# Optimization experiments

Hardware: AMD Instinct MI355X
Metric: run time of the kernel (lower is better)

## Reference

```python
import jax, jax.numpy as jnp
from jax import lax
import numpy as np

B, L, D_MODEL = 4, 2048, 1024
D_INNER = 2 * D_MODEL          # expand=2
N = 16                          # d_state
DCONV = 4                       # d_conv
DTRANK = D_MODEL // 16          # dt_rank = 64
DFF = 4 * D_MODEL               # 4096


def setup_inputs() -> dict:
    key = jax.random.key(0)
    ks = jax.random.split(key, 10)
    def g(i, shape, scale=0.02):
        return jax.random.normal(ks[i], shape, jnp.float32) * scale
    return {
        "x": jax.random.normal(ks[0], (B, L, D_MODEL), jnp.float32),
        # Mamba params (mamba_ssm defaults: in_proj/x_proj/out_proj no bias)
        "in_proj_w": g(1, (2 * D_INNER, D_MODEL)),
        "conv_w": g(2, (D_INNER, 1, DCONV), 0.1),
        "conv_b": jnp.zeros((D_INNER,), jnp.float32),
        "x_proj_w": g(3, (DTRANK + 2 * N, D_INNER)),
        "dt_proj_w": g(4, (D_INNER, DTRANK), 0.1),
        # inverse-softplus of ~0.01 so softplus(dt) starts small, as in Mamba init
        "dt_proj_b": jnp.log(jnp.expm1(jnp.full((D_INNER,), 1e-2, jnp.float32))),
        "A_log": jnp.log(jnp.broadcast_to(jnp.arange(1, N + 1, dtype=jnp.float32), (D_INNER, N))),
        "D": jnp.ones((D_INNER,), jnp.float32),
        "out_proj_w": g(5, (D_MODEL, D_INNER)),
        # FFN params (nn.Linear has bias)
        "lin1_w": g(6, (DFF, D_MODEL)),
        "lin1_b": jnp.zeros((DFF,), jnp.float32),
        "lin2_w": g(7, (D_MODEL, DFF)),
        "lin2_b": jnp.zeros((D_MODEL,), jnp.float32),
    }


def _mamba(x, in_proj_w, conv_w, conv_b, x_proj_w, dt_proj_w, dt_proj_b,
           A_log, D, out_proj_w):
    Bb = x.shape[0]
    xz = jnp.einsum('bld,ed->ble', x, in_proj_w)        # [B,L,2*d_inner]
    u, z = jnp.split(xz, 2, axis=-1)                    # each [B,L,d_inner]
    # causal depthwise conv1d over time
    uc = jnp.transpose(u, (0, 2, 1))                    # [B,d_inner,L]
    uc = lax.conv_general_dilated(uc, conv_w, (1,), [(DCONV - 1, 0)],
                                  feature_group_count=D_INNER)
    uc = jax.nn.silu(uc + conv_b[None, :, None])
    u = jnp.transpose(uc, (0, 2, 1))                    # [B,L,d_inner]
    # input-dependent dt, B, C
    x_dbl = jnp.einsum('ble,fe->blf', u, x_proj_w)      # [B,L,dt_rank+2N]
    dt, Bm, Cm = jnp.split(x_dbl, [DTRANK, DTRANK + N], axis=-1)
    dt = jax.nn.softplus(jnp.einsum('blr,er->ble', dt, dt_proj_w) + dt_proj_b)
    A = -jnp.exp(A_log)                                 # [d_inner,N]

    def step(h, inputs):
        u_t, dt_t, B_t, C_t = inputs                    # [B,E],[B,E],[B,N],[B,N]
        dA = jnp.exp(dt_t[..., None] * A)               # [B,E,N]
        h = dA * h + (dt_t * u_t)[..., None] * B_t[:, None, :]
        y = jnp.einsum('ben,bn->be', h, C_t)
        return h, y

    h0 = jnp.zeros((Bb, D_INNER, N), x.dtype)
    xs = (jnp.transpose(u, (1, 0, 2)), jnp.transpose(dt, (1, 0, 2)),
          jnp.transpose(Bm, (1, 0, 2)), jnp.transpose(Cm, (1, 0, 2)))
    _, ys = lax.scan(step, h0, xs)                      # ys: [L,B,d_inner]
    y = jnp.transpose(ys, (1, 0, 2)) + u * D
    y = y * jax.nn.silu(z)
    return jnp.einsum('ble,de->bld', y, out_proj_w)     # [B,L,d_model]


def reference(x, in_proj_w, conv_w, conv_b, x_proj_w, dt_proj_w, dt_proj_b,
              A_log, D, out_proj_w, lin1_w, lin1_b, lin2_w, lin2_b):
    y = _mamba(x, in_proj_w, conv_w, conv_b, x_proj_w, dt_proj_w, dt_proj_b,
               A_log, D, out_proj_w)
    h = jax.nn.relu(jnp.einsum('bld,fd->blf', y, lin1_w) + lin1_b)
    return jnp.einsum('blf,df->bld', h, lin2_w) + lin2_b
```

## Files before the change

### kernel.cpp

```cpp
#include <hip/hip_runtime.h>
#include <hip/hip_bf16.h>
#include <type_traits>
#include <math.h>

typedef __hip_bfloat16 bf16_t;

#define BB 4
#define LL 2048
#define DM 1024
#define DI 2048
#define NS 16
#define DTR 64
#define DFF 4096
#define MTOK (BB*LL)
#define NC 32
#define CL (LL/NC)
#define TT 16
#define KS 4

#if defined(__has_builtin)
#if __has_builtin(__builtin_amdgcn_exp2f)
#define EXP2F(x) __builtin_amdgcn_exp2f(x)
#endif
#endif
#ifndef EXP2F
#define EXP2F(x) exp2f(x)
#endif
#define LOG2E 1.44269504088896340736f

__device__ __forceinline__ float b2f_lo(unsigned u) {
    union { unsigned x; float f; } c; c.x = u << 16; return c.f;
}
__device__ __forceinline__ float b2f_hi(unsigned u) {
    union { unsigned x; float f; } c; c.x = u & 0xffff0000u; return c.f;
}
__device__ __forceinline__ void unpack8(uint4 v, float* o) {
    o[0] = b2f_lo(v.x); o[1] = b2f_hi(v.x);
    o[2] = b2f_lo(v.y); o[3] = b2f_hi(v.y);
    o[4] = b2f_lo(v.z); o[5] = b2f_hi(v.z);
    o[6] = b2f_lo(v.w); o[7] = b2f_hi(v.w);
}

typedef __attribute__((ext_vector_type(8))) short bf16x8;
typedef __attribute__((ext_vector_type(4))) float f32x4;

__device__ __forceinline__ void gld_lds16(const void* g, void* l) {
    __builtin_amdgcn_global_load_lds(
        (const __attribute__((address_space(1))) void*)g,
        (__attribute__((address_space(3))) void*)l, 16, 0, 0);
}

#define G8_BAR  __builtin_amdgcn_s_barrier()
#define G8_SB   __builtin_amdgcn_sched_barrier(0)
#define G8_LGKM do { asm volatile("s_waitcnt lgkmcnt(0)" ::: "memory"); G8_SB; } while (0)
#define G8_VM8  do { asm volatile("s_waitcnt vmcnt(8)"   ::: "memory"); G8_SB; } while (0)
#define G8_VM6  do { asm volatile("s_waitcnt vmcnt(6)"   ::: "memory"); G8_SB; } while (0)
#define G8_VM4  do { asm volatile("s_waitcnt vmcnt(4)"   ::: "memory"); G8_SB; } while (0)
#define G8_VM2  do { asm volatile("s_waitcnt vmcnt(2)"   ::: "memory"); G8_SB; } while (0)
#define G8_VM0  do { asm volatile("s_waitcnt vmcnt(0)"   ::: "memory"); G8_SB; } while (0)

__global__ void detect_dtype_kernel(const unsigned* __restrict__ x, int* __restrict__ flag)
{
    __shared__ int cnt;
    if (threadIdx.x == 0) cnt = 0;
    __syncthreads();
    int c = 0;
    for (int i = threadIdx.x; i < 4096; i += 256) {
        unsigned w = x[i];
        int e = (w >> 7) & 0xFF;
        c += (e >= 100 && e <= 140) ? 1 : 0;
    }
    atomicAdd(&cnt, c);
    __syncthreads();
    if (threadIdx.x == 0) *flag = (cnt > 2048) ? 1 : 0;
}

struct CvtDesc {
    const void* src[14];
    bf16_t*     dst[14];
    int         cum[15];
};

__global__ __launch_bounds__(256)
void convert_all(CvtDesc d, const int* __restrict__ flag, int total8)
{
    int i = blockIdx.x * 256 + threadIdx.x;
    if (i >= total8) return;
    int t = 0;
#pragma unroll 1
    while (i >= d.cum[t + 1]) ++t;
    int j = i - d.cum[t];
    if (*flag) {
        ((uint4*)d.dst[t])[j] = ((const uint4*)d.src[t])[j];
    } else {
        const float4* s = (const float4*)d.src[t] + (size_t)j * 2;
        float4 a = s[0], b = s[1];
        bf16_t o[8];
        o[0] = __float2bfloat16(a.x); o[1] = __float2bfloat16(a.y);
        o[2] = __float2bfloat16(a.z); o[3] = __float2bfloat16(a.w);
        o[4] = __float2bfloat16(b.x); o[5] = __float2bfloat16(b.y);
        o[6] = __float2bfloat16(b.z); o[7] = __float2bfloat16(b.w);
        ((uint4*)d.dst[t])[j] = *(uint4*)o;
    }
}

#define G8_NK 16

template <int EPI, bool SPLIT>
__global__ __launch_bounds__(512, 2)
void gemm8(const bf16_t* __restrict__ A, const bf16_t* __restrict__ W,
           bf16_t* __restrict__ C, bf16_t* __restrict__ C2,
           const bf16_t* __restrict__ bias, int ldc)
{
    __shared__ __align__(16) bf16_t ldsmem[2][2][256 * 64];

    const int tid  = threadIdx.x;
    const int lane = tid & 63;
    const int wv   = tid >> 6;
    const int wm   = wv >> 2;
    const int wn   = wv & 3;
    const int r16  = lane & 15;
    const int q    = lane >> 4;
    const int m0   = blockIdx.x * 256;
    const int n0   = blockIdx.y * 256;

    const int x0 = q ^ (r16 & 7);
    const int x1 = (4 + q) ^ (r16 & 7);

    const int srow = tid >> 3;
    const int scol = (tid & 7) ^ (srow & 7);
    const bf16_t* Abase = A + (size_t)(m0 + srow) * 1024 + scol * 8;
    const bf16_t* Wbase = W + (size_t)(n0 + srow) * 1024 + scol * 8;
    const int woff = wv * 1024;

    const bf16x8* L8 = (const bf16x8*)ldsmem;
    char*         Lb = (char*)ldsmem;

    f32x4  acc[8][4] = {};
    bf16x8 af[4][2];
    bf16x8 bfr[2][2][2];

    auto stA = [&](int bufc, int tile, int half) {
        const bf16_t* g = Abase + (size_t)half * (128 * 1024) + tile * 64;
        char* l = Lb + (size_t)(bufc * 2 + 0) * 32768 + half * 16384 + woff;
        gld_lds16(g, l);
        gld_lds16(g + 64 * 1024, l + 8192);
    };
    auto stB = [&](int bufc, int tile, int half) {
        const bf16_t* g = Wbase + (size_t)half * (128 * 1024) + tile * 64;
        char* l = Lb + (size_t)(bufc * 2 + 1) * 32768 + half * 16384 + woff;
        gld_lds16(g, l);
        gld_lds16(g + 64 * 1024, l + 8192);
    };
    auto rdA = [&](int bufc, int mh) {
#pragma unroll
        for (int mf = 0; mf < 4; ++mf) {
            int rb = (bufc * 2 + 0) * 2048 + (wm * 128 + mh * 64 + mf * 16 + r16) * 8;
            af[mf][0] = L8[rb + x0];
            af[mf][1] = L8[rb + x1];
        }
    };
    auto rdB = [&](int bufc, int nh) {
#pragma unroll
        for (int nf = 0; nf < 2; ++nf) {
            int rb = (bufc * 2 + 1) * 2048 + (wn * 64 + nh * 32 + nf * 16 + r16) * 8;
            bfr[nh][nf][0] = L8[rb + x0];
            bfr[nh][nf][1] = L8[rb + x1];
        }
    };
    auto mmQ = [&](int mh, int nh) {
#pragma unroll
        for (int mf = 0; mf < 4; ++mf)
#pragma unroll
            for (int nf = 0; nf < 2; ++nf) {
                acc[mh*4+mf][nh*2+nf] = __builtin_amdgcn_mfma_f32_16x16x32_bf16(
                    af[mf][0], bfr[nh][nf][0], acc[mh*4+mf][nh*2+nf], 0, 0, 0);
                acc[mh*4+mf][nh*2+nf] = __builtin_amdgcn_mfma_f32_16x16x32_bf16(
                    af[mf][1], bfr[nh][nf][1], acc[mh*4+mf][nh*2+nf], 0, 0, 0);
            }
    };

#define G8_PH(mh, nh) do { G8_BAR; G8_LGKM;                      \
        __builtin_amdgcn_s_setprio(1); mmQ(mh, nh);              \
        __builtin_amdgcn_s_setprio(0); G8_SB; G8_BAR; G8_SB; } while (0)

    stA(0, 0, 0); stA(0, 0, 1);
    stB(0, 0, 0); stB(0, 0, 1);
    stB(1, 1, 0); stB(1, 1, 1);
    G8_VM4;
    G8_BAR; G8_SB;

    for (int i = 0; i < G8_NK / 2 - 1; ++i) {
        const int v1 = 2 * i + 1, u2 = 2 * i + 2, v2 = 2 * i + 3;
        rdA(0,0); rdB(0,0); stA(1, v1, 0);         G8_PH(0,0);
        rdB(0,1);           stA(1, v1, 1);         G8_PH(0,1);
        rdA(0,1);           stB(0, u2, 0);         G8_PH(1,0);
                            stB(0, u2, 1); G8_VM4; G8_PH(1,1);
        rdA(1,0); rdB(1,0); stA(0, u2, 0);         G8_PH(0,0);
        rdB(1,1);           stA(0, u2, 1);         G8_PH(0,1);
        rdA(1,1);           stB(1, v2, 0);         G8_PH(1,0);
                            stB(1, v2, 1); G8_VM4; G8_PH(1,1);
    }
    rdA(0,0); rdB(0,0); stA(1, G8_NK - 1, 0); G8_PH(0,0);
    rdB(0,1);           stA(1, G8_NK - 1, 1); G8_PH(0,1);
    rdA(0,1);                                 G8_PH(1,0);
                        G8_VM0;               G8_PH(1,1);
    rdA(1,0); rdB(1,0);                       G8_PH(0,0);
    rdB(1,1);                                 G8_PH(0,1);
    rdA(1,1);                                 G8_PH(1,0);
                                              G8_PH(1,1);

    bf16_t* Cb = C;
    int csub = 0;
    if (SPLIT && n0 >= 2048) { Cb = C2; csub = 2048; }
#pragma unroll
    for (int b = 0; b < 4; ++b) {
        int colg = n0 + wn * 64 + (b >> 1) * 32 + (b & 1) * 16 + r16;
        float bv = 0.f;
        if (EPI >= 1) bv = __bfloat162float(bias[colg]);
#pragma unroll
        for (int a = 0; a < 8; ++a) {
#pragma unroll
            for (int r = 0; r < 4; ++r) {
                int rowg = m0 + wm * 128 + (a >> 2) * 64 + (a & 3) * 16 + q * 4 + r;
                float v = acc[a][b][r];
                if (EPI >= 1) v += bv;
                if (EPI == 2) v = v > 0.f ? v : 0.f;
                Cb[(size_t)rowg * ldc + (colg - csub)] = __float2bfloat16(v);
            }
        }
    }
#undef G8_PH
}

template <int LDK, int NKT, int EPI, bool DYN>
__global__ __launch_bounds__(512, 2)
void gemm8n(const bf16_t* __restrict__ A, const bf16_t* __restrict__ W,
            bf16_t* __restrict__ C, const bf16_t* __restrict__ bias, int ldc,
            const int* oflag, int c_row_off)
{
    __shared__ __align__(16) bf16_t ldsmem[2][24576];

    const int tid  = threadIdx.x;
    const int lane = tid & 63;
    const int wv   = tid >> 6;
    const int wm   = wv >> 2;
    const int wn   = wv & 3;
    const int r16  = lane & 15;
    const int q    = lane >> 4;
    const int m0   = blockIdx.x * 256;
    const int n0   = blockIdx.y * 128;

    const int x0 = q ^ (r16 & 7);
    const int x1 = (4 + q) ^ (r16 & 7);

    const int srow = tid >> 3;
    const int scol = (tid & 7) ^ (srow & 7);
    const bf16_t* Abase = A + (size_t)(m0 + srow) * LDK + scol * 8;
    const bf16_t* Wbase = W + (size_t)(n0 + srow) * LDK + scol * 8;
    const int woff = wv * 1024;

    const bf16x8* L8 = (const bf16x8*)ldsmem;
    char*         Lb = (char*)ldsmem;

    f32x4  acc[8][2] = {};
    bf16x8 af[4][2];
    bf16x8 bfr[2][2];

    auto stA = [&](int bufc, int tile, int half) {
        const bf16_t* g = Abase + (size_t)half * (128 * LDK) + tile * 64;
        char* l = Lb + (size_t)bufc * 49152 + half * 16384 + woff;
        gld_lds16(g, l);
        gld_lds16(g + (size_t)64 * LDK, l + 8192);
    };
    auto stB = [&](int bufc, int tile) {
        const bf16_t* g = Wbase + tile * 64;
        char* l = Lb + (size_t)bufc * 49152 + 32768 + woff;
        gld_lds16(g, l);
        gld_lds16(g + (size_t)64 * LDK, l + 8192);
    };
    auto rdA = [&](int bufc, int mh) {
#pragma unroll
        for (int mf = 0; mf < 4; ++mf) {
            int rb = bufc * 3072 + (wm * 128 + mh * 64 + mf * 16 + r16) * 8;
            af[mf][0] = L8[rb + x0];
            af[mf][1] = L8[rb + x1];
        }
    };
    auto rdB = [&](int bufc) {
#pragma unroll
        for (int nf = 0; nf < 2; ++nf) {
            int rb = bufc * 3072 + 2048 + (wn * 32 + nf * 16 + r16) * 8;
            bfr[nf][0] = L8[rb + x0];
            bfr[nf][1] = L8[rb + x1];
        }
    };
    auto mmP = [&](int mh) {
#pragma unroll
        for (int mf = 0; mf < 4; ++mf)
#pragma unroll
            for (int nf = 0; nf < 2; ++nf) {
                acc[mh*4+mf][nf] = __builtin_amdgcn_mfma_f32_16x16x32_bf16(
                    af[mf][0], bfr[nf][0], acc[mh*4+mf][nf], 0, 0, 0);
                acc[mh*4+mf][nf] = __builtin_amdgcn_mfma_f32_16x16x32_bf16(
                    af[mf][1], bfr[nf][1], acc[mh*4+mf][nf], 0, 0, 0);
            }
    };

#define GN_PH(mh) do { G8_BAR; G8_LGKM;                          \
        __builtin_amdgcn_s_setprio(1); mmP(mh);                  \
        __builtin_amdgcn_s_setprio(0); G8_SB; G8_BAR; G8_SB; } while (0)

    stA(0, 0, 0); stA(0, 0, 1);
    stB(0, 0);
    stB(1, 1);
    G8_VM2;
    G8_BAR; G8_SB;

    for (int i = 0; i < NKT / 2 - 1; ++i) {
        const int v1 = 2 * i + 1, u2 = 2 * i + 2, v2 = 2 * i + 3;
        rdA(0,0); rdB(0); stA(1, v1, 0); stA(1, v1, 1); GN_PH(0);
        rdA(0,1);         stB(0, u2); G8_VM2;           GN_PH(1);
        rdA(1,0); rdB(1); stA(0, u2, 0); stA(0, u2, 1); GN_PH(0);
        rdA(1,1);         stB(1, v2); G8_VM2;           GN_PH(1);
    }
    rdA(0,0); rdB(0); stA(1, NKT - 1, 0); stA(1, NKT - 1, 1); GN_PH(0);
    rdA(0,1);         G8_VM0;                                 GN_PH(1);
    rdA(1,0); rdB(1);                                         GN_PH(0);
    rdA(1,1);                                                 GN_PH(1);

    int of = 1;
    if constexpr (DYN) of = *oflag;
#pragma unroll
    for (int nf = 0; nf < 2; ++nf) {
        int colg = n0 + wn * 32 + nf * 16 + r16;
        float bv = 0.f;
        if (EPI >= 1) bv = __bfloat162float(bias[colg]);
#pragma unroll
        for (int a = 0; a < 8; ++a) {
#pragma unroll
            for (int r = 0; r < 4; ++r) {
                int rowg = m0 + wm * 128 + a * 16 + q * 4 + r;
                float v = acc[a][nf][r];
                if (EPI >= 1) v += bv;
                if constexpr (DYN) {
                    size_t idx = (size_t)(c_row_off + rowg) * ldc + colg;
                    if (of) ((bf16_t*)C)[idx] = __float2bfloat16(v);
                    else    ((float*)C)[idx]  = v;
                } else {
                    C[(size_t)rowg * ldc + colg] = __float2bfloat16(v);
                }
            }
        }
    }
#undef GN_PH
}

#define TM 128
#define TN 128
#define TK 64

template <typename OutT, int EPI, bool DYN, bool EDGE>
__global__ __launch_bounds__(256, 2)
void gemm_bt(const bf16_t* __restrict__ A, int lda,
             const bf16_t* __restrict__ W, int ldw,
             OutT* __restrict__ C, int ldc,
             OutT* __restrict__ C2, int nsplit,
             const bf16_t* __restrict__ bias,
             int M, int N, int K,
             const int* oflag, int c_row_off)
{
    __shared__ bf16_t sA[TM * TK];
    __shared__ bf16_t sB[TN * TK];

    const int tid  = threadIdx.x;
    const int lane = tid & 63;
    const int wv   = tid >> 6;
    const int m0   = blockIdx.x * TM;
    const int n0   = blockIdx.y * TN;
    const int wm   = (wv >> 1) * 64;
    const int wn   = (wv & 1) * 64;
    const int r16  = lane & 15;
    const int q    = lane >> 4;

    int of = 1;
    if constexpr (DYN) of = *oflag;

    f32x4 acc[4][4] = {};

    for (int k0 = 0; k0 < K; k0 += TK) {
#pragma unroll
        for (int i = 0; i < 4; ++i) {
            int c    = (i * 4 + wv) * 64 + lane;
            int row  = c >> 3;
            int col8 = c & 7;
            const bf16_t* ga = A + (size_t)(m0 + row) * lda + k0 + col8 * 8;
            gld_lds16(ga, (char*)sA + (size_t)(i * 4 + wv) * 1024);
            int nrow = n0 + row;
            if (EDGE && nrow > N - 1) nrow = N - 1;
            const bf16_t* gb = W + (size_t)nrow * ldw + k0 + col8 * 8;
            gld_lds16(gb, (char*)sB + (size_t)(i * 4 + wv) * 1024);
        }
        __syncthreads();

        const bf16x8* sA8 = (const bf16x8*)sA;
        const bf16x8* sB8 = (const bf16x8*)sB;
#pragma unroll
        for (int kk = 0; kk < 2; ++kk) {
            bf16x8 af[4], bfr[4];
#pragma unroll
            for (int i = 0; i < 4; ++i)
                af[i] = sA8[(wm + i * 16 + r16) * 8 + kk * 4 + q];
#pragma unroll
            for (int j = 0; j < 4; ++j)
                bfr[j] = sB8[(wn + j * 16 + r16) * 8 + kk * 4 + q];
#pragma unroll
            for (int i = 0; i < 4; ++i)
#pragma unroll
                for (int j = 0; j < 4; ++j)
                    acc[i][j] = __builtin_amdgcn_mfma_f32_16x16x32_bf16(
                        af[i], bfr[j], acc[i][j], 0, 0, 0);
        }
        __syncthreads();
    }

    OutT* Cb = C;
    int csub = 0;
    if (C2 != nullptr && n0 >= nsplit) { Cb = C2; csub = nsplit; }

#pragma unroll
    for (int j = 0; j < 4; ++j) {
        int colg = n0 + wn + j * 16 + r16;
        if (EDGE && colg >= N) continue;
        float bv = 0.f;
        if (EPI >= 1) bv = __bfloat162float(bias[colg]);
#pragma unroll
        for (int i = 0; i < 4; ++i) {
#pragma unroll
            for (int r = 0; r < 4; ++r) {
                int rowg = m0 + wm + i * 16 + q * 4 + r;
                if (EDGE && rowg >= M) continue;
                float v = acc[i][j][r];
                if (EPI >= 1) v += bv;
                if (EPI == 2) v = v > 0.f ? v : 0.f;
                if (EPI == 3) v = (v > 20.f) ? v : log1pf(__expf(v));
                if constexpr (DYN) {
                    size_t idx = (size_t)(c_row_off + rowg) * ldc + colg;
                    if (of) ((bf16_t*)Cb)[idx] = __float2bfloat16(v);
                    else    ((float*)Cb)[idx]  = v;
                } else if constexpr (std::is_same<OutT, float>::value) {
                    Cb[(size_t)rowg * ldc + (colg - csub)] = v;
                } else {
                    Cb[(size_t)rowg * ldc + (colg - csub)] = __float2bfloat16(v);
                }
            }
        }
    }
}

__global__ __launch_bounds__(256, 2)
void gemm_xproj_splitk(const bf16_t* __restrict__ A,
                       const bf16_t* __restrict__ W,
                       float* __restrict__ part, int M)
{
    __shared__ bf16_t sA[TM * TK];
    __shared__ bf16_t sB[TN * TK];

    const int tid  = threadIdx.x;
    const int lane = tid & 63;
    const int wv   = tid >> 6;
    const int m0   = blockIdx.x * TM;
    const int kz   = blockIdx.z;
    const int wm   = (wv >> 1) * 64;
    const int wn   = (wv & 1) * 64;
    const int r16  = lane & 15;
    const int q    = lane >> 4;

    f32x4 acc[4][4] = {};

    const int kbeg = kz * (2048 / KS);
    for (int k0 = kbeg; k0 < kbeg + 2048 / KS; k0 += TK) {
#pragma unroll
        for (int i = 0; i < 4; ++i) {
            int c    = (i * 4 + wv) * 64 + lane;
            int row  = c >> 3;
            int col8 = c & 7;
            const bf16_t* ga = A + (size_t)(m0 + row) * DI + k0 + col8 * 8;
            gld_lds16(ga, (char*)sA + (size_t)(i * 4 + wv) * 1024);
            int nrow = row; if (nrow > 95) nrow = 95;
            const bf16_t* gb = W + (size_t)nrow * DI + k0 + col8 * 8;
            gld_lds16(gb, (char*)sB + (size_t)(i * 4 + wv) * 1024);
        }
        __syncthreads();

        const bf16x8* sA8 = (const bf16x8*)sA;
        const bf16x8* sB8 = (const bf16x8*)sB;
#pragma unroll
        for (int kk = 0; kk < 2; ++kk) {
            bf16x8 af[4], bfr[4];
#pragma unroll
            for (int i = 0; i < 4; ++i)
                af[i] = sA8[(wm + i * 16 + r16) * 8 + kk * 4 + q];
#pragma unroll
            for (int j = 0; j < 4; ++j)
                bfr[j] = sB8[(wn + j * 16 + r16) * 8 + kk * 4 + q];
#pragma unroll
            for (int i = 0; i < 4; ++i)
#pragma unroll
                for (int j = 0; j < 4; ++j)
                    acc[i][j] = __builtin_amdgcn_mfma_f32_16x16x32_bf16(
                        af[i], bfr[j], acc[i][j], 0, 0, 0);
        }
        __syncthreads();
    }

#pragma unroll
    for (int j = 0; j < 4; ++j) {
        int colg = wn + j * 16 + r16;
        if (colg >= 96) continue;
#pragma unroll
        for (int i = 0; i < 4; ++i) {
#pragma unroll
            for (int r = 0; r < 4; ++r) {
                int rowg = m0 + wm + i * 16 + q * 4 + r;
                part[((size_t)kz * M + rowg) * 96 + colg] = acc[i][j][r];
            }
        }
    }
}

__global__ __launch_bounds__(256)
void xproj_reduce(const float* __restrict__ part, bf16_t* __restrict__ xdbl,
                  float* __restrict__ x32, int M)
{
    int i = blockIdx.x * 256 + threadIdx.x;
    int n = M * 96;
    if (i >= n) return;
    float s = part[i] + part[(size_t)n + i] + part[2 * (size_t)n + i] + part[3 * (size_t)n + i];
    xdbl[i] = __float2bfloat16(s);
    if (x32) x32[i] = s;
}

__global__ __launch_bounds__(256)
void conv_silu_kernel(const bf16_t* __restrict__ u,
                      const bf16_t* __restrict__ cw,
                      const bf16_t* __restrict__ cb,
                      bf16_t* __restrict__ uc,
                      int Mrows)
{
    int idx = blockIdx.x * 256 + threadIdx.x;
    int eg  = idx & 255;
    int row = idx >> 8;
    if (row >= Mrows) return;
    int t = row & (LL - 1);
    int b = row >> 11;
    int e0 = eg * 8;

    float wf[32];
    {
        const uint4* wp = (const uint4*)(cw + (size_t)e0 * 4);
        uint4 w0 = wp[0], w1 = wp[1], w2 = wp[2], w3 = wp[3];
        unpack8(w0, wf); unpack8(w1, wf + 8); unpack8(w2, wf + 16); unpack8(w3, wf + 24);
    }
    float bias[8];
    unpack8(*(const uint4*)(cb + e0), bias);

    float uk[4][8];
#pragma unroll
    for (int k = 0; k < 4; ++k) {
        int tt = t - 3 + k;
        if (tt >= 0) {
            uint4 uv = *(const uint4*)(u + (size_t)(b * LL + tt) * DI + e0);
            unpack8(uv, uk[k]);
        } else {
#pragma unroll
            for (int j = 0; j < 8; ++j) uk[k][j] = 0.f;
        }
    }
    bf16_t out8[8];
#pragma unroll
    for (int j = 0; j < 8; ++j) {
        float a = bias[j];
#pragma unroll
        for (int k = 0; k < 4; ++k) a += wf[j * 4 + k] * uk[k][j];
        a = a / (1.f + __expf(-a));
        out8[j] = __float2bfloat16(a);
    }
    *(uint4*)(uc + (size_t)row * DI + e0) = *(uint4*)out8;
}


__global__ __launch_bounds__(256, 4)
void scan_pass1(const bf16_t* __restrict__ uc, const bf16_t* __restrict__ dtb,
                const float* __restrict__ x32, const bf16_t* __restrict__ A_log,
                float* __restrict__ hfin, float* __restrict__ Ssum, int lgG)
{
    __shared__ __align__(16) char sm1[36864];
    const int tid  = threadIdx.x;
    const int lane = tid & 63;
    const int wv   = tid >> 6;
    const int bid  = blockIdx.x;
    const int eb   = bid & 7;
    const int rem  = bid >> 3;
    const int b    = rem & ((1 << lgG) - 1);
    const int chunk = rem >> lgG;
    const int e0   = eb * 256;
    const int e    = e0 + tid;
    const int t0   = chunk * CL;

    const bf16_t* ub = uc  + (size_t)(b * LL + t0) * DI;
    const bf16_t* db = dtb + (size_t)(b * LL + t0) * DI;
    const float*  xr = x32 + (size_t)(b * LL + t0) * 96 + 64;

    char* const U[2] = { sm1, sm1 + 8192 };
    char* const D[2] = { sm1 + 16384, sm1 + 24576 };
    char* const Bl   = sm1 + 32768;

    auto stage2 = [&](const bf16_t* src, char* dst, int trow0) {
        const int c8 = (lane & 31) * 8;
        const int r0 = 2 * wv + (lane >> 5);
        gld_lds16(src + (size_t)(trow0 + r0) * DI + e0 + c8, dst + wv * 1024 + lane * 16);
        gld_lds16(src + (size_t)(trow0 + r0 + 8) * DI + e0 + c8, dst + (wv + 4) * 1024 + lane * 16);
    };
    {
        int s = tid >> 2, p = tid & 3;
        gld_lds16(xr + (size_t)s * 96 + p * 4, Bl + tid * 16);
    }
    stage2(ub, U[0], 0);  stage2(db, D[0], 0);
    stage2(ub, U[1], TT); stage2(db, D[1], TT);

    float alf[16];
    {
        uint4 v0 = *(const uint4*)(A_log + (size_t)e * NS);
        uint4 v1 = *(const uint4*)(A_log + (size_t)e * NS + 8);
        unpack8(v0, alf); unpack8(v1, alf + 8);
    }
    float a0 = -__expf(alf[0]) * LOG2E;
    float Aa2[16];
    int fast = 1;
#pragma unroll
    for (int n = 0; n < 16; ++n) {
        Aa2[n] = -__expf(alf[n]) * LOG2E;
        float ideal = (float)(n + 1) * a0;
        fast = fast && (fabsf(Aa2[n] - ideal) <= 0.02f * fabsf(ideal));
    }
    int allfast = __syncthreads_and(fast);

    float h[16];
#pragma unroll
    for (int j = 0; j < 16; ++j) h[j] = 0.f;
    float Ss = 0.f;

#define P1_CMP(K, FAST) do {                                                  \
        const char* Ut = U[(K) & 1]; const char* Dt = D[(K) & 1];             \
        _Pragma("unroll")                                                     \
        for (int t = 0; t < TT; ++t) {                                        \
            float cu  = __bfloat162float(*(const bf16_t*)(Ut + t * 512 + tid * 2)); \
            float cdt = __bfloat162float(*(const bf16_t*)(Dt + t * 512 + tid * 2)); \
            const float* bc = (const float*)(Bl + ((K) * TT + t) * 64);       \
            float du = cdt * cu; Ss += cdt;                                   \
            if (FAST) {                                                       \
                float r = EXP2F(cdt * a0);                                    \
                float r2 = r * r, r4 = r2 * r2, r8 = r4 * r4;                 \
                float dA = r, dB = r8 * r;                                    \
                _Pragma("unroll")                                             \
                for (int j = 0; j < 8; ++j) { h[j] = dA * h[j] + du * bc[j]; dA *= r; } \
                _Pragma("unroll")                                             \
                for (int j = 8; j < 16; ++j) { h[j] = dB * h[j] + du * bc[j]; dB *= r; } \
            } else {                                                          \
                _Pragma("unroll")                                             \
                for (int j = 0; j < 16; ++j) {                                \
                    float dA = EXP2F(cdt * Aa2[j]);                           \
                    h[j] = dA * h[j] + du * bc[j]; }                          \
            }                                                                 \
        } } while (0)

#define P1_SEQ(FAST) do {                                                     \
        G8_VM4; G8_BAR; G8_SB;                                                \
        P1_CMP(0, FAST); G8_LGKM; G8_BAR; G8_SB;                              \
        stage2(ub, U[0], 2 * TT); stage2(db, D[0], 2 * TT);                   \
        G8_VM4; G8_BAR; G8_SB;                                                \
        P1_CMP(1, FAST); G8_LGKM; G8_BAR; G8_SB;                              \
        stage2(ub, U[1], 3 * TT); stage2(db, D[1], 3 * TT);                   \
        G8_VM4; G8_BAR; G8_SB;                                                \
        P1_CMP(2, FAST); G8_LGKM; G8_BAR; G8_SB;                              \
        G8_VM0; G8_BAR; G8_SB;                                                \
        P1_CMP(3, FAST);                                                      \
    } while (0)

    if (allfast) P1_SEQ(true); else P1_SEQ(false);
#undef P1_SEQ
#undef P1_CMP

    size_t base = (size_t)(b * NC + chunk) * NS * DI + e;
#pragma unroll
    for (int j = 0; j < 16; ++j) hfin[base + (size_t)j * DI] = h[j];
    Ssum[(size_t)(b * NC + chunk) * DI + e] = Ss;
}

__global__ __launch_bounds__(256)
void scan_pass2(const float* __restrict__ Ssum, const bf16_t* __restrict__ A_log,
                float* __restrict__ hfin)
{
    int idx = blockIdx.x * 256 + threadIdx.x;
    int e = idx & (DI - 1);
    int rem = idx >> 11;
    int n = rem & (NS - 1);
    int b = rem >> 4;
    float Aa2 = -__expf(__bfloat162float(A_log[(size_t)e * NS + n])) * LOG2E;
    float h = 0.f;
    for (int c = 0; c < NC; ++c) {
        size_t a = ((size_t)(b * NC + c) * NS + n) * DI + e;
        float S  = Ssum[(size_t)(b * NC + c) * DI + e];
        float hf = hfin[a];
        hfin[a] = h;
        h = EXP2F(Aa2 * S) * h + hf;
    }
}

__global__ __launch_bounds__(256, 2)
void scan_pass3(const bf16_t* __restrict__ uc, const bf16_t* __restrict__ dtb,
                const float* __restrict__ x32, bf16_t* __restrict__ zy,
                const bf16_t* __restrict__ A_log, const bf16_t* __restrict__ Dp,
                const float* __restrict__ hin, int lgG)
{
    __shared__ __align__(16) char sm3[65536];
    const int tid  = threadIdx.x;
    const int lane = tid & 63;
    const int wv   = tid >> 6;
    const int bid  = blockIdx.x;
    const int eb   = bid & 7;
    const int rem  = bid >> 3;
    const int b    = rem & ((1 << lgG) - 1);
    const int chunk = rem >> lgG;
    const int e0   = eb * 256;
    const int e    = e0 + tid;
    const int t0   = chunk * CL;

    const bf16_t* ub = uc  + (size_t)(b * LL + t0) * DI;
    const bf16_t* db = dtb + (size_t)(b * LL + t0) * DI;
    bf16_t*       zb = zy  + (size_t)(b * LL + t0) * DI;
    const float*  xr = x32 + (size_t)(b * LL + t0) * 96 + 64;

    char* const U[2] = { sm3, sm3 + 8192 };
    char* const D[2] = { sm3 + 16384, sm3 + 24576 };
    char* const Z[2] = { sm3 + 32768, sm3 + 40960 };
    char* const Y    = sm3 + 49152;
    char* const BC   = sm3 + 57344;

    auto stage2 = [&](const bf16_t* src, char* dst, int trow0) {
        const int c8 = (lane & 31) * 8;
        const int r0 = 2 * wv + (lane >> 5);
        gld_lds16(src + (size_t)(trow0 + r0) * DI + e0 + c8, dst + wv * 1024 + lane * 16);
        gld_lds16(src + (size_t)(trow0 + r0 + 8) * DI + e0 + c8, dst + (wv + 4) * 1024 + lane * 16);
    };
    {
        int s1 = tid >> 3, p1 = tid & 7;
        gld_lds16(xr + (size_t)s1 * 96 + p1 * 4, BC + tid * 16);
        gld_lds16(xr + (size_t)(s1 + 32) * 96 + p1 * 4, BC + 4096 + tid * 16);
    }
    stage2(ub, U[0], 0);  stage2(db, D[0], 0);  stage2(zb, Z[0], 0);
    stage2(ub, U[1], TT); stage2(db, D[1], TT); stage2(zb, Z[1], TT);

    float alf[16];
    {
        uint4 v0 = *(const uint4*)(A_log + (size_t)e * NS);
        uint4 v1 = *(const uint4*)(A_log + (size_t)e * NS + 8);
        unpack8(v0, alf); unpack8(v1, alf + 8);
    }
    float a0 = -__expf(alf[0]) * LOG2E;
    float Aa2[16];
    int fast = 1;
#pragma unroll
    for (int n = 0; n < 16; ++n) {
        Aa2[n] = -__expf(alf[n]) * LOG2E;
        float ideal = (float)(n + 1) * a0;
        fast = fast && (fabsf(Aa2[n] - ideal) <= 0.02f * fabsf(ideal));
    }
    int allfast = __syncthreads_and(fast);

    float Dv = __bfloat162float(Dp[e]);
    size_t hbase = (size_t)(b * NC + chunk) * NS * DI + e;
    float h[16];
#pragma unroll
    for (int j = 0; j < 16; ++j) h[j] = hin[hbase + (size_t)j * DI];

    auto yflush = [&](int K) {
        const int r0 = tid >> 5;
        const int c  = (tid & 31) * 16;
        uint4 v0 = *(const uint4*)(Y + r0 * 512 + c);
        uint4 v1 = *(const uint4*)(Y + (r0 + 8) * 512 + c);
        *(uint4*)(zb + (size_t)(K * TT + r0) * DI + e0 + (tid & 31) * 8)     = v0;
        *(uint4*)(zb + (size_t)(K * TT + r0 + 8) * DI + e0 + (tid & 31) * 8) = v1;
    };

#define P3_CMP(K, FAST) do {                                                  \
        const char* Ut = U[(K) & 1]; const char* Dt = D[(K) & 1];             \
        const char* Zt = Z[(K) & 1];                                          \
        _Pragma("unroll")                                                     \
        for (int t = 0; t < TT; ++t) {                                        \
            float cu  = __bfloat162float(*(const bf16_t*)(Ut + t * 512 + tid * 2)); \
            float cdt = __bfloat162float(*(const bf16_t*)(Dt + t * 512 + tid * 2)); \
            float cz  = __bfloat162float(*(const bf16_t*)(Zt + t * 512 + tid * 2)); \
            const float* bc = (const float*)(BC + ((K) * TT + t) * 128);      \
            float du = cdt * cu;                                              \
            if (FAST) {                                                       \
                float r = EXP2F(cdt * a0);                                    \
                float r2 = r * r, r4 = r2 * r2, r8 = r4 * r4;                 \
                float dA = r, dB = r8 * r;                                    \
                _Pragma("unroll")                                             \
                for (int j = 0; j < 8; ++j) { h[j] = dA * h[j] + du * bc[j]; dA *= r; } \
                _Pragma("unroll")                                             \
                for (int j = 8; j < 16; ++j) { h[j] = dB * h[j] + du * bc[j]; dB *= r; } \
            } else {                                                          \
                _Pragma("unroll")                                             \
                for (int j = 0; j < 16; ++j) {                                \
                    float dA = EXP2F(cdt * Aa2[j]);                           \
                    h[j] = dA * h[j] + du * bc[j]; }                          \
            }                                                                 \
            float y1 = 0.f, y2 = 0.f;                                         \
            _Pragma("unroll")                                                 \
            for (int j = 0; j < 8; ++j)  y1 += h[j] * bc[16 + j];             \
            _Pragma("unroll")                                                 \
            for (int j = 8; j < 16; ++j) y2 += h[j] * bc[16 + j];             \
            float yv  = y1 + y2;                                              \
            float sil = cz / (1.f + __expf(-cz));                             \
            *(bf16_t*)(Y + t * 512 + tid * 2) =                               \
                __float2bfloat16((yv + cu * Dv) * sil);                       \
        } } while (0)

#define P3_SEQ(FAST) do {                                                     \
        G8_VM6; G8_BAR; G8_SB;                                                \
        P3_CMP(0, FAST); G8_LGKM; G8_BAR; G8_SB;                              \
        yflush(0);                                                            \
        stage2(ub, U[0], 2*TT); stage2(db, D[0], 2*TT); stage2(zb, Z[0], 2*TT); \
        G8_VM8; G8_BAR; G8_SB;                                                \
        P3_CMP(1, FAST); G8_LGKM; G8_BAR; G8_SB;                              \
        yflush(1);                                                            \
        stage2(ub, U[1], 3*TT); stage2(db, D[1], 3*TT); stage2(zb, Z[1], 3*TT); \
        G8_VM8; G8_BAR; G8_SB;                                                \
        P3_CMP(2, FAST); G8_LGKM; G8_BAR; G8_SB;                              \
        yflush(2);                                                            \
        G8_VM2; G8_BAR; G8_SB;                                                \
        P3_CMP(3, FAST); G8_LGKM; G8_BAR; G8_SB;                              \
        yflush(3);                                                            \
    } while (0)

    if (allfast) P3_SEQ(true); else P3_SEQ(false);
#undef P3_SEQ
#undef P3_CMP
}

__global__ __launch_bounds__(64)
void scan_kernel(const bf16_t* __restrict__ uc,
                 const bf16_t* __restrict__ dt,
                 const bf16_t* __restrict__ xdbl,
                 bf16_t* __restrict__ zy,
                 const bf16_t* __restrict__ A_log,
                 const bf16_t* __restrict__ Dp)
{
    int idx = blockIdx.x * 64 + threadIdx.x;
    int e = idx & (DI - 1);
    int b = idx >> 11;

    float Aa[NS];
#pragma unroll
    for (int n = 0; n < NS; ++n)
        Aa[n] = -__expf(__bfloat162float(A_log[e * NS + n]));
    float Dv = __bfloat162float(Dp[e]);
    float h[NS];
#pragma unroll
    for (int n = 0; n < NS; ++n) h[n] = 0.f;

    const bf16_t* up  = uc   + (size_t)b * LL * DI + e;
    const bf16_t* dp  = dt   + (size_t)b * LL * DI + e;
    const bf16_t* zp  = zy   + (size_t)b * LL * DI + e;
    const bf16_t* bcp = xdbl + (size_t)b * LL * 96 + 64;
    bf16_t*       yp  = zy   + (size_t)b * LL * DI + e;

    float nu  = __bfloat162float(*up);
    float ndt = __bfloat162float(*dp);
    float nz  = __bfloat162float(*zp);
    uint4 nb0 = *(const uint4*)(bcp);
    uint4 nb1 = *(const uint4*)(bcp + 8);
    uint4 nc0 = *(const uint4*)(bcp + 16);
    uint4 nc1 = *(const uint4*)(bcp + 24);

    for (int t = 0; t < LL; ++t) {
        float cu = nu, cdt = ndt, cz = nz;
        uint4 b0 = nb0, b1 = nb1, c0 = nc0, c1 = nc1;
        if (t + 1 < LL) {
            up += DI; dp += DI; zp += DI; bcp += 96;
            nu  = __bfloat162float(*up);
            ndt = __bfloat162float(*dp);
            nz  = __bfloat162float(*zp);
            nb0 = *(const uint4*)(bcp);
            nb1 = *(const uint4*)(bcp + 8);
            nc0 = *(const uint4*)(bcp + 16);
            nc1 = *(const uint4*)(bcp + 24);
        }
        float Bv[NS], Cv[NS];
        unpack8(b0, Bv); unpack8(b1, Bv + 8);
        unpack8(c0, Cv); unpack8(c1, Cv + 8);

        float du = cdt * cu;
        float yv = 0.f;
#pragma unroll
        for (int n = 0; n < NS; ++n) {
            float dA = __expf(cdt * Aa[n]);
            h[n] = dA * h[n] + du * Bv[n];
            yv += h[n] * Cv[n];
        }
        float sil  = cz / (1.f + __expf(-cz));
        float outv = (yv + cu * Dv) * sil;
        *yp = __float2bfloat16(outv);
        yp += DI;
    }
}

extern "C" void kernel_launch(void* const* d_in, const int* in_sizes, int n_in,
                              void* d_out, int out_size, void* d_ws, size_t ws_size,
                              hipStream_t stream)
{
    char* ws = (char*)d_ws;
    int* flag = (int*)ws;
    size_t cur = 256;
    auto alloc = [&](size_t bytes) { bf16_t* p = (bf16_t*)(ws + cur); cur += bytes; return p; };

    const size_t o_xb = cur;
    bf16_t* xb   = alloc((size_t)MTOK * DM * 2);
    bf16_t* w_in = alloc((size_t)2 * DI * DM * 2);
    bf16_t* w_o  = alloc((size_t)DM * DI * 2);
    bf16_t* w_l1 = alloc((size_t)DFF * DM * 2);
    bf16_t* w_l2 = alloc((size_t)DM * DFF * 2);
    bf16_t* w_xp = alloc((size_t)96 * DI * 2);
    bf16_t* w_dt = alloc((size_t)DI * DTR * 2);
    bf16_t* cw   = alloc((size_t)DI * 4 * 2);
    bf16_t* cb   = alloc((size_t)DI * 2);
    bf16_t* dpb  = alloc((size_t)DI * 2);
    bf16_t* alog = alloc((size_t)DI * NS * 2);
    bf16_t* dd   = alloc((size_t)DI * 2);
    bf16_t* l1b  = alloc((size_t)DFF * 2);
    bf16_t* l2b  = alloc((size_t)DM * 2 + 2048);
    cur = (cur + 255) & ~(size_t)255;
    const size_t o_pipe = cur;

    detect_dtype_kernel<<<1, 256, 0, stream>>>((const unsigned*)d_in[0], flag);

    {
        CvtDesc d;
        const void* ss[14] = { d_in[0], d_in[1], d_in[9], d_in[10], d_in[12], d_in[4],
                               d_in[5], d_in[2], d_in[3], d_in[6], d_in[7], d_in[8],
                               d_in[11], d_in[13] };
        bf16_t* dd_[14]    = { xb, w_in, w_o, w_l1, w_l2, w_xp,
                               w_dt, cw, cb, dpb, alog, dd, l1b, l2b };
        size_t  nn[14]     = { (size_t)MTOK*DM, (size_t)2*DI*DM, (size_t)DM*DI,
                               (size_t)DFF*DM, (size_t)DM*DFF, (size_t)96*DI,
                               (size_t)DI*DTR, (size_t)DI*4, (size_t)DI, (size_t)DI,
                               (size_t)DI*NS, (size_t)DI, (size_t)DFF, (size_t)DM };
        int c = 0; d.cum[0] = 0;
        for (int i = 0; i < 14; ++i) {
            d.src[i] = ss[i]; d.dst[i] = dd_[i];
            c += (int)(nn[i] / 8); d.cum[i + 1] = c;
        }
        convert_all<<<(c + 255) / 256, 256, 0, stream>>>(d, flag, c);
    }

    auto pipe = [&](int Gq) { return (size_t)Gq * LL * 96 * 2 + 3ull * Gq * LL * DI * 2; };
    auto scr  = [&](int Gq) {
        return (size_t)Gq * NC * NS * DI * 4 + (size_t)Gq * NC * DI * 4 + (size_t)Gq * LL * 96 * 4;
    };

    int G; bool chunked; size_t scr_off;
    if      (ws_size >= o_pipe + pipe(4))            { G = 4; chunked = true;  scr_off = o_xb; }
    else if (ws_size >= o_pipe + pipe(2) + scr(2))   { G = 2; chunked = true;  scr_off = o_pipe + pipe(2); }
    else if (ws_size >= o_pipe + pipe(1) + scr(1))   { G = 1; chunked = true;  scr_off = o_pipe + pipe(1); }
    else                                             { G = 1; chunked = false; scr_off = o_pipe + pipe(1); }
    const int lgG = (G == 4) ? 2 : (G == 2 ? 1 : 0);

    const size_t hfin_sz = (size_t)G * NC * NS * DI * 4;
    const size_t ssum_sz = (size_t)G * NC * DI * 4;

    for (int g0 = 0; g0 < BB; g0 += G) {
        const int    Mg      = G * LL;
        const size_t xdbl_sz = (size_t)Mg * 96 * 2;
        const size_t big     = (size_t)Mg * DI * 2;

        bf16_t* xdbl = (bf16_t*)(ws + o_pipe);
        bf16_t* ubuf = (bf16_t*)(ws + o_pipe + xdbl_sz);
        bf16_t* dtb  = ubuf;
        bf16_t* zbuf = (bf16_t*)(ws + o_pipe + xdbl_sz + big);
        bf16_t* uc   = (bf16_t*)(ws + o_pipe + xdbl_sz + 2 * big);
        bf16_t* my   = uc;
        bf16_t* hh   = (bf16_t*)(ws + o_pipe);
        float*  xpp  = (float*)(ws + scr_off);
        float*  x32  = chunked ? (float*)(ws + scr_off + hfin_sz + ssum_sz) : nullptr;

        const bf16_t* x_g = xb + (size_t)g0 * LL * DM;

        dim3 blk(256);
        const int gx = Mg / TM;

        gemm8<0, true><<<dim3(Mg / 256, 16), 512, 0, stream>>>(
            x_g, w_in, ubuf, zbuf, nullptr, DI);
        conv_silu_kernel<<<Mg, 256, 0, stream>>>(ubuf, cw, cb, uc, Mg);
        gemm_xproj_splitk<<<dim3(gx, 1, KS), blk, 0, stream>>>(uc, w_xp, xpp, Mg);
        xproj_reduce<<<(Mg * 96 + 255) / 256, 256, 0, stream>>>(xpp, xdbl, x32, Mg);
        gemm_bt<bf16_t, 3, false, false><<<dim3(gx, DI / TN), blk, 0, stream>>>(
            xdbl, 96, w_dt, DTR, dtb, DI, nullptr, 0, dpb, Mg, DI, DTR, nullptr, 0);
        if (chunked) {
            float* hfin = (float*)(ws + scr_off);
            float* Ssum = (float*)(ws + scr_off + hfin_sz);
            scan_pass1<<<G * NC * (DI / 256), 256, 0, stream>>>(uc, dtb, x32, alog, hfin, Ssum, lgG);
            scan_pass2<<<G * (NS * DI / 256), 256, 0, stream>>>(Ssum, alog, hfin);
            scan_pass3<<<G * NC * (DI / 256), 256, 0, stream>>>(uc, dtb, x32, zbuf, alog, dd, hfin, lgG);
        } else {
            scan_kernel<<<(G * DI) / 64, 64, 0, stream>>>(uc, dtb, xdbl, zbuf, alog, dd);
        }
        gemm8n<2048, 32, 0, false><<<dim3(Mg / 256, DM / 128), 512, 0, stream>>>(
            zbuf, w_o, my, nullptr, DM, nullptr, 0);
        gemm8<2, false><<<dim3(Mg / 256, 16), 512, 0, stream>>>(
            my, w_l1, hh, nullptr, l1b, DFF);
        gemm8n<4096, 64, 1, true><<<dim3(Mg / 256, DM / 128), 512, 0, stream>>>(
            hh, w_l2, (bf16_t*)d_out, l2b, DM, (const int*)ws, g0 * LL);
    }
}
```

Measured before the change: 630.8 us.

## Remap GEMM tiles across XCDs and stage gemm8 epilogue through LDS

Both GEMM kernels now remap the linear block index so that consecutive blocks, which are dispatched round-robin across the 8 XCDs, land on neighbouring tiles. The aim is better L2 reuse of A and W within each XCD. gemm8's epilogue now writes the bf16 results into a padded LDS tile, one 128-row half at a time, then stores full rows to global memory with 16-byte vector stores instead of scattered 2-byte stores. This adds barriers and LDS traffic, and the padded row stride produces 16-byte LDS reads that are not 16-byte aligned.

```diff
diff --git a/kernel.cpp b/kernel.cpp
--- a/kernel.cpp
+++ b/kernel.cpp
@@ -121,8 +121,12 @@
     const int wn   = wv & 3;
     const int r16  = lane & 15;
     const int q    = lane >> 4;
-    const int m0   = blockIdx.x * 256;
-    const int n0   = blockIdx.y * 256;
+
+    const int lin = blockIdx.y * gridDim.x + blockIdx.x;
+    const int per = (gridDim.x * gridDim.y) >> 3;
+    const int l2  = (lin & 7) * per + (lin >> 3);
+    const int m0  = (l2 % gridDim.x) * 256;
+    const int n0  = (l2 / gridDim.x) * 256;
 
     const int x0 = q ^ (r16 & 7);
     const int x1 = (4 + q) ^ (r16 & 7);
@@ -213,22 +217,42 @@
     bf16_t* Cb = C;
     int csub = 0;
     if (SPLIT && n0 >= 2048) { Cb = C2; csub = 2048; }
-#pragma unroll
-    for (int b = 0; b < 4; ++b) {
-        int colg = n0 + wn * 64 + (b >> 1) * 32 + (b & 1) * 16 + r16;
-        float bv = 0.f;
-        if (EPI >= 1) bv = __bfloat162float(bias[colg]);
-#pragma unroll
-        for (int a = 0; a < 8; ++a) {
-#pragma unroll
-            for (int r = 0; r < 4; ++r) {
-                int rowg = m0 + wm * 128 + (a >> 2) * 64 + (a & 3) * 16 + q * 4 + r;
-                float v = acc[a][b][r];
-                if (EPI >= 1) v += bv;
-                if (EPI == 2) v = v > 0.f ? v : 0.f;
-                Cb[(size_t)rowg * ldc + (colg - csub)] = __float2bfloat16(v);
+
+    bf16_t* T = (bf16_t*)ldsmem;
+#pragma unroll
+    for (int h = 0; h < 2; ++h) {
+        if (wm == h) {
+#pragma unroll
+            for (int b = 0; b < 4; ++b) {
+                int col = wn * 64 + (b >> 1) * 32 + (b & 1) * 16 + r16;
+                float bv = 0.f;
+                if (EPI >= 1) bv = __bfloat162float(bias[n0 + col]);
+#pragma unroll
+                for (int a = 0; a < 8; ++a) {
+#pragma unroll
+                    for (int r = 0; r < 4; ++r) {
+                        int lr = (a >> 2) * 64 + (a & 3) * 16 + q * 4 + r;
+                        float v = acc[a][b][r];
+                        if (EPI >= 1) v += bv;
+                        if (EPI == 2) v = v > 0.f ? v : 0.f;
+                        T[lr * 258 + col] = __float2bfloat16(v);
+                    }
+                }
             }
         }
+        __syncthreads();
+        {
+            int row = tid >> 2, qt = tid & 3;
+            int rowg = m0 + h * 128 + row;
+            const char* src = (const char*)T + row * 516 + qt * 128;
+            char* dstg = (char*)(Cb + (size_t)rowg * ldc + (n0 - csub) + qt * 64);
+#pragma unroll
+            for (int k = 0; k < 8; ++k) {
+                uint4 v = *(const uint4*)(src + k * 16);
+                *(uint4*)(dstg + k * 16) = v;
+            }
+        }
+        __syncthreads();
     }
 #undef G8_PH
 }
@@ -248,8 +272,12 @@
     const int wn   = wv & 3;
     const int r16  = lane & 15;
     const int q    = lane >> 4;
-    const int m0   = blockIdx.x * 256;
-    const int n0   = blockIdx.y * 128;
+
+    const int lin = blockIdx.y * gridDim.x + blockIdx.x;
+    const int per = (gridDim.x * gridDim.y) >> 3;
+    const int l2  = (lin & 7) * per + (lin >> 3);
+    const int m0  = (l2 % gridDim.x) * 256;
+    const int n0  = (l2 / gridDim.x) * 128;
 
     const int x0 = q ^ (r16 & 7);
     const int x1 = (4 + q) ^ (r16 & 7);
@@ -588,7 +616,6 @@
     }
     *(uint4*)(uc + (size_t)row * DI + e0) = *(uint4*)out8;
 }
-
 
 __global__ __launch_bounds__(256, 4)
 void scan_pass1(const bf16_t* __restrict__ uc, const bf16_t* __restrict__ dtb,
```

New measurement: 679.7 us. 7.8% more time.
